# Optimization experiments

Measured on AMD Instinct MI355X. Metric: run time of the kernel, lower is better.

Reference implementation:

```python
import jax, jax.numpy as jnp
import numpy as np

B, S, C = 4, 4096, 1024
H, D, K = 16, 64, 256  # nhead, head_dim, dim_k


def setup_inputs() -> dict:
    key = jax.random.key(0)
    ks = jax.random.split(key, 7)
    x = jax.random.normal(ks[0], (B, S, C), dtype=jnp.float32)
    # per-head QKV projection weights (torch Linear weight layout [out,in])
    Wq = jax.random.normal(ks[1], (H, D, C), dtype=jnp.float32) * (C ** -0.5)
    Wk = jax.random.normal(ks[2], (H, D, C), dtype=jnp.float32) * (C ** -0.5)
    Wv = jax.random.normal(ks[3], (H, D, C), dtype=jnp.float32) * (C ** -0.5)
    # Linformer E/F sequence projections, per head: [K, S]
    We = jax.random.normal(ks[4], (H, K, S), dtype=jnp.float32) * (S ** -0.5)
    Wf = jax.random.normal(ks[5], (H, K, S), dtype=jnp.float32) * (S ** -0.5)
    # output projection (with bias, as w_o is nn.Linear default bias=True)
    Wo = jax.random.normal(ks[6], (C, H * D), dtype=jnp.float32) * ((H * D) ** -0.5)
    bo = jnp.zeros((C,), dtype=jnp.float32)
    return {"x": x, "Wq": Wq, "Wk": Wk, "Wv": Wv, "We": We, "Wf": Wf, "Wo": Wo, "bo": bo}


def reference(x, Wq, Wk, Wv, We, Wf, Wo, bo):
    # per-head projections: [B,H,S,D]
    Q = jnp.einsum('bsc,hdc->bhsd', x, Wq)
    Kh = jnp.einsum('bsc,hdc->bhsd', x, Wk)
    Vh = jnp.einsum('bsc,hdc->bhsd', x, Wv)
    # E-projection of K over the sequence axis: K^T [B,H,D,S] -> [B,H,D,K]
    Kp = jnp.einsum('bhsd,hks->bhdk', Kh, We)
    # scores: Q @ E(K^T) / sqrt(head_dim), softmax over low-rank axis k
    scale = 1.0 / jnp.sqrt(jnp.asarray(D, dtype=x.dtype))
    P = jax.nn.softmax(jnp.einsum('bhsd,bhdk->bhsk', Q, Kp) * scale, axis=-1)
    # F-projection of V over the sequence axis, then transpose back: [B,H,K,D]
    Vp = jnp.einsum('bhsd,hks->bhkd', Vh, Wf)
    out = jnp.einsum('bhsk,bhkd->bhsd', P, Vp)          # [B,H,S,D]
    out = out.transpose(0, 2, 1, 3).reshape(B, S, H * D)  # concat heads
    return jnp.einsum('bse,ce->bsc', out, Wo) + bo       # w_o (dropout=0)
```

## Files before the change

### kernel.cpp

```cpp
#include <hip/hip_runtime.h>
#include <stdint.h>


typedef unsigned short u16;
typedef __bf16 bf16t;
typedef bf16t bf16x8 __attribute__((ext_vector_type(8)));
typedef float f32x4 __attribute__((ext_vector_type(4)));
typedef u16 u16x8 __attribute__((ext_vector_type(8)));

#define MFMA16(a, b, c) __builtin_amdgcn_mfma_f32_16x16x32_bf16((a), (b), (c), 0, 0, 0)

__device__ __forceinline__ u16 f2bf(float f) {
  return __builtin_bit_cast(u16, (bf16t)f);
}

__device__ __forceinline__ bf16x8 ldf(const u16* p) { return *(const bf16x8*)p; }

__device__ __forceinline__ void gload16(const void* g, void* l) {
  __builtin_amdgcn_global_load_lds(
      (__attribute__((address_space(1))) void*)g,
      (__attribute__((address_space(3))) void*)l, 16, 0, 0);
}

__device__ __forceinline__ int xcd_swz(int orig, int nwg) {
  return (orig & 7) * (nwg >> 3) + (orig >> 3);
}

__device__ __forceinline__ void gemm256_pipe(const u16* __restrict__ A,
                                             const u16* __restrict__ B,
                                             int m0, int n0, int sA1, int sB1,
                                             int s0, int kt0, f32x4 acc[8][4],
                                             char* smc) {
  const int tid = threadIdx.x;
  const int w = tid >> 6, l = tid & 63, g = l >> 4, r = l & 15;
  const int wr = w >> 2, wc = w & 3;
  const int lrow = l >> 2;
  const int ksw = (((l & 3) ^ ((l >> 3) & 3)) << 4);
  const int gx = ((g ^ ((r >> 1) & 3)) << 4);

  auto stage = [&](const u16* Base, int r0, int s1, int T, int ch, int ldsoff) {
#pragma unroll
    for (int i = 0; i < 2; ++i) {
      const int row = r0 + (w * 2 + i) * 16 + lrow;
      const size_t eoff = (size_t)(row >> 6) * s1 + (size_t)(row & 63) * s0;
      gload16((const char*)Base + eoff * 2 + ((kt0 + T) * 64 + ch * 32) * 2 + ksw,
              smc + ldsoff + (w * 2 + i) * 1024);
    }
  };

  stage(A, m0, sA1, 0, 0, 0);
  stage(B, n0, sB1, 0, 0, 32768);
  stage(A, m0, sA1, 0, 1, 16384);
  stage(B, n0, sB1, 0, 1, 32768 + 16384);

  for (int t = 0; t < 16; ++t) {
    const int buf = (t & 1) << 16, nb = buf ^ 65536;
    const int Tn = t < 15 ? t + 1 : 15;
    bf16x8 af[4], bfv[4];

#define QUAD(MH)                                                        \
  __builtin_amdgcn_s_setprio(1);                                        \
  _Pragma("unroll") for (int m = 0; m < 4; ++m)                         \
      _Pragma("unroll") for (int n = 0; n < 4; ++n)                     \
          acc[(MH)*4 + m][n] = MFMA16(af[m], bfv[n], acc[(MH)*4 + m][n]); \
  __builtin_amdgcn_s_setprio(0);

    stage(A, m0, sA1, Tn, 0, nb);
    asm volatile("s_waitcnt vmcnt(6)" ::: "memory");
    __builtin_amdgcn_s_barrier();
    asm volatile("" ::: "memory");
    {
      const char* At = smc + buf;
      const char* Bt = smc + buf + 32768;
#pragma unroll
      for (int n = 0; n < 4; ++n)
        bfv[n] = *(const bf16x8*)(Bt + (wc * 64 + n * 16 + r) * 64 + gx);
#pragma unroll
      for (int m = 0; m < 4; ++m)
        af[m] = *(const bf16x8*)(At + (wr * 128 + m * 16 + r) * 64 + gx);
      QUAD(0)
      stage(B, n0, sB1, Tn, 0, nb + 32768);
#pragma unroll
      for (int m = 0; m < 4; ++m)
        af[m] = *(const bf16x8*)(At + (wr * 128 + 64 + m * 16 + r) * 64 + gx);
      QUAD(1)
    }
    stage(A, m0, sA1, Tn, 1, nb + 16384);
    asm volatile("s_waitcnt vmcnt(6)" ::: "memory");
    __builtin_amdgcn_s_barrier();
    asm volatile("" ::: "memory");
    {
      const char* At = smc + buf + 16384;
      const char* Bt = smc + buf + 32768 + 16384;
#pragma unroll
      for (int n = 0; n < 4; ++n)
        bfv[n] = *(const bf16x8*)(Bt + (wc * 64 + n * 16 + r) * 64 + gx);
#pragma unroll
      for (int m = 0; m < 4; ++m)
        af[m] = *(const bf16x8*)(At + (wr * 128 + m * 16 + r) * 64 + gx);
      QUAD(0)
      stage(B, n0, sB1, Tn, 1, nb + 32768 + 16384);
#pragma unroll
      for (int m = 0; m < 4; ++m)
        af[m] = *(const bf16x8*)(At + (wr * 128 + 64 + m * 16 + r) * 64 + gx);
      QUAD(1)
    }
#undef QUAD
  }
}

__global__ __launch_bounds__(256) void cvt_x(const float* __restrict__ src,
                                             u16* __restrict__ dst) {
  const size_t i = ((size_t)blockIdx.x * 256 + threadIdx.x) * 8;
  const float4 a = *(const float4*)(src + i);
  const float4 b = *(const float4*)(src + i + 4);
  u16x8 o;
  o[0] = f2bf(a.x); o[1] = f2bf(a.y); o[2] = f2bf(a.z); o[3] = f2bf(a.w);
  o[4] = f2bf(b.x); o[5] = f2bf(b.y); o[6] = f2bf(b.z); o[7] = f2bf(b.w);
  *(u16x8*)(dst + i) = o;
}

__global__ __launch_bounds__(256) void cvt_w(const float* __restrict__ Wq,
                                             const float* __restrict__ Wk,
                                             const float* __restrict__ Wv,
                                             const float* __restrict__ Wo,
                                             u16* __restrict__ wqkv,
                                             u16* __restrict__ wob) {
  const float* s;
  u16* d;
  switch (blockIdx.y) {
    case 0: s = Wq; d = wqkv; break;
    case 1: s = Wk; d = wqkv + 1048576; break;
    case 2: s = Wv; d = wqkv + 2097152; break;
    default: s = Wo; d = wob; break;
  }
  const size_t i = ((size_t)blockIdx.x * 256 + threadIdx.x) * 8;
  const float4 a = *(const float4*)(s + i);
  const float4 b = *(const float4*)(s + i + 4);
  u16x8 o;
  o[0] = f2bf(a.x); o[1] = f2bf(a.y); o[2] = f2bf(a.z); o[3] = f2bf(a.w);
  o[4] = f2bf(b.x); o[5] = f2bf(b.y); o[6] = f2bf(b.z); o[7] = f2bf(b.w);
  *(u16x8*)(d + i) = o;
}

__global__ __launch_bounds__(256) void cvt_wef(const float* __restrict__ We,
                                               const float* __restrict__ Wf,
                                               u16* __restrict__ web,
                                               u16* __restrict__ wfb) {
  const float* s = blockIdx.y ? Wf : We;
  u16* d = blockIdx.y ? wfb : web;
  const size_t i = ((size_t)blockIdx.x * 256 + threadIdx.x) * 8;
  const float4 a = *(const float4*)(s + i);
  const float4 b = *(const float4*)(s + i + 4);
  u16x8 o;
  o[0] = f2bf(a.x); o[1] = f2bf(a.y); o[2] = f2bf(a.z); o[3] = f2bf(a.w);
  o[4] = f2bf(b.x); o[5] = f2bf(b.y); o[6] = f2bf(b.z); o[7] = f2bf(b.w);
  *(u16x8*)(d + i) = o;
}

__global__ __launch_bounds__(512, 2) void gemm_q(const u16* __restrict__ A,
                                                 const u16* __restrict__ BT,
                                                 u16* __restrict__ Qd) {
  __shared__ u16 sm[65536];
  const int wg = xcd_swz(blockIdx.x, 256);
  const int m0 = (wg >> 2) * 256, n0 = (wg & 3) * 256;
  const int tid = threadIdx.x, w = tid >> 6, l = tid & 63, g = l >> 4, r = l & 15;
  const int wr = w >> 2, wc = w & 3;
  f32x4 acc[8][4] = {};
  gemm256_pipe(A, BT, m0, n0, 65536, 65536, 1024, 0, acc, (char*)sm);
#pragma unroll
  for (int m = 0; m < 8; ++m)
#pragma unroll
    for (int n = 0; n < 4; ++n)
#pragma unroll
      for (int j = 0; j < 4; ++j) {
        const int mm = m0 + wr * 128 + m * 16 + g * 4 + j;
        const int nn = n0 + wc * 64 + n * 16 + r;
        const int b = mm >> 12, s = mm & 4095, h = nn >> 6, d = nn & 63;
        Qd[(((size_t)(b * 16 + h)) * 4096 + s) * 64 + d] = f2bf(acc[m][n][j] * 0.125f);
      }
}

__global__ __launch_bounds__(512, 2) void gemm_kv(const u16* __restrict__ A,
                                                  const u16* __restrict__ BT,
                                                  u16* __restrict__ KTd,
                                                  u16* __restrict__ VTd) {
  __shared__ u16 sm[65536];
  const int wg = xcd_swz(blockIdx.x, 512);
  const int m0 = (wg & 7) * 256, n0 = (wg >> 3) * 256;
  const int tid = threadIdx.x, w = tid >> 6, l = tid & 63, g = l >> 4, r = l & 15;
  const int wr = w >> 2, wc = w & 3;
  f32x4 acc[8][4] = {};
  gemm256_pipe(A, BT, m0, n0, 65536, 65536, 1024, 0, acc, (char*)sm);
#pragma unroll
  for (int m = 0; m < 8; ++m)
#pragma unroll
    for (int n = 0; n < 4; ++n)
#pragma unroll
      for (int j = 0; j < 4; ++j) {
        const int mm = m0 + wr * 128 + m * 16 + g * 4 + j;
        const int nn = n0 + wc * 64 + n * 16 + r;
        const int which = mm >> 10, hd = mm & 1023, h = hd >> 6, d = hd & 63;
        const int b = nn >> 12, s = nn & 4095;
        u16* dst = which ? VTd : KTd;
        dst[(((size_t)(b * 16 + h)) * 64 + d) * 4096 + s] = f2bf(acc[m][n][j]);
      }
}

__global__ __launch_bounds__(512, 2) void gemm_out(const u16* __restrict__ A,
                                                   const u16* __restrict__ BT,
                                                   const float* __restrict__ bo,
                                                   float* __restrict__ out) {
  __shared__ u16 sm[65536];
  const int wg = xcd_swz(blockIdx.x, 256);
  const int m0 = (wg >> 2) * 256, n0 = (wg & 3) * 256;
  const int tid = threadIdx.x, w = tid >> 6, l = tid & 63, g = l >> 4, r = l & 15;
  const int wr = w >> 2, wc = w & 3;
  f32x4 acc[8][4] = {};
  gemm256_pipe(A, BT, m0, n0, 65536, 65536, 1024, 0, acc, (char*)sm);
#pragma unroll
  for (int m = 0; m < 8; ++m)
#pragma unroll
    for (int n = 0; n < 4; ++n)
#pragma unroll
      for (int j = 0; j < 4; ++j) {
        const int mm = m0 + wr * 128 + m * 16 + g * 4 + j;
        const int nn = n0 + wc * 64 + n * 16 + r;
        out[(size_t)mm * 1024 + nn] = acc[m][n][j] + bo[nn];
      }
}

__global__ __launch_bounds__(512, 2) void gemm_small(const u16* __restrict__ web,
                                                     const u16* __restrict__ wfb,
                                                     const u16* __restrict__ KT,
                                                     const u16* __restrict__ VT,
                                                     float* __restrict__ part) {
  __shared__ u16 sm[65536];
  const int bx = blockIdx.x;
  const int h = bx & 15, mode = (bx >> 4) & 1, chunk = bx >> 5;
  const u16 *Ab, *Bb;
  int sA1, sB1;
  if (mode == 0) {
    Ab = web + (size_t)h * 1048576; sA1 = 262144;
    Bb = KT + (size_t)h * 262144;   sB1 = 4194304;
  } else {
    Ab = VT + (size_t)h * 262144;   sA1 = 4194304;
    Bb = wfb + (size_t)h * 1048576; sB1 = 262144;
  }
  f32x4 acc[8][4] = {};
  gemm256_pipe(Ab, Bb, 0, 0, sA1, sB1, 4096, chunk * 16, acc, (char*)sm);
  float* Cp = part + ((size_t)((mode * 4 + chunk) * 16 + h)) * 65536;
  const int tid = threadIdx.x, w = tid >> 6, l = tid & 63, g = l >> 4, r = l & 15;
  const int wr = w >> 2, wc = w & 3;
#pragma unroll
  for (int m = 0; m < 8; ++m)
#pragma unroll
    for (int n = 0; n < 4; ++n)
#pragma unroll
      for (int j = 0; j < 4; ++j)
        Cp[(size_t)(wr * 128 + m * 16 + g * 4 + j) * 256 + wc * 64 + n * 16 + r] =
            acc[m][n][j];
}

__global__ __launch_bounds__(256) void reduce_small(const float* __restrict__ part,
                                                    u16* __restrict__ Kp,
                                                    u16* __restrict__ VpT) {
  const int i = blockIdx.x * 256 + threadIdx.x;
  const int mode = i >> 18;
  const int rem = i & 262143;
  const int h = rem >> 14;
  const int e = (rem & 16383) * 4;
  const int m = e >> 8, n = e & 255;
  const float* pb = part + ((size_t)mode * 64 + h) * 65536 + e;
  const float4 s0 = *(const float4*)(pb);
  const float4 s1 = *(const float4*)(pb + 1048576);
  const float4 s2 = *(const float4*)(pb + 2097152);
  const float4 s3 = *(const float4*)(pb + 3145728);
  ushort4 o;
  o.x = f2bf(s0.x + s1.x + s2.x + s3.x);
  o.y = f2bf(s0.y + s1.y + s2.y + s3.y);
  o.z = f2bf(s0.z + s1.z + s2.z + s3.z);
  o.w = f2bf(s0.w + s1.w + s2.w + s3.w);
  if (mode == 0) {
    const int b = n >> 6, d = n & 63;
    *(ushort4*)(Kp + ((size_t)(b * 16 + h)) * 16384 + m * 64 + d) = o;
  } else {
    const int b = m >> 6, d = m & 63;
    *(ushort4*)(VpT + ((size_t)(b * 16 + h)) * 16384 + d * 256 + n) = o;
  }
}

__global__ __launch_bounds__(256, 1) void attn_fused(const u16* __restrict__ Q,
                                                     const u16* __restrict__ Kp,
                                                     const u16* __restrict__ VpT,
                                                     u16* __restrict__ att) {
  __shared__ u16 P[4][16 * 264];
  const int gid = blockIdx.x;
  const int bh = gid >> 3;
  const int st = gid & 7;
  const int hh = bh & 15, b = bh >> 4;
  const int tid = threadIdx.x, w = tid >> 6, l = tid & 63, g = l >> 4, r = l & 15;
  const u16* Kpb = Kp + (size_t)bh * 256 * 64;
  const u16* Vb = VpT + (size_t)bh * 64 * 256;

  bf16x8 kf[32];
  bf16x8 vf[32];
#pragma unroll
  for (int fn = 0; fn < 16; ++fn) {
    kf[fn * 2 + 0] = ldf(Kpb + (fn * 16 + r) * 64 + g * 8);
    kf[fn * 2 + 1] = ldf(Kpb + (fn * 16 + r) * 64 + 32 + g * 8);
  }
#pragma unroll
  for (int fn2 = 0; fn2 < 4; ++fn2)
#pragma unroll
    for (int kk = 0; kk < 8; ++kk)
      vf[fn2 * 8 + kk] = ldf(Vb + (fn2 * 16 + r) * 256 + kk * 32 + g * 8);

  u16* Pw = P[w];
  for (int t = 0; t < 8; ++t) {
    const int s0 = st * 512 + t * 64 + w * 16;
    const u16* Qb = Q + ((size_t)bh * 4096 + s0) * 64;
    const bf16x8 qf0 = ldf(Qb + r * 64 + g * 8);
    const bf16x8 qf1 = ldf(Qb + r * 64 + 32 + g * 8);
    f32x4 sc[16];
#pragma unroll
    for (int fn = 0; fn < 16; ++fn) {
      sc[fn] = MFMA16(qf0, kf[fn * 2 + 0], (f32x4){});
      sc[fn] = MFMA16(qf1, kf[fn * 2 + 1], sc[fn]);
    }
    float rinv[4];
#pragma unroll
    for (int j = 0; j < 4; ++j) {
      float sum = 0.f;
#pragma unroll
      for (int fn = 0; fn < 16; ++fn) {
        const float e = __expf(sc[fn][j]);
        sc[fn][j] = e;
        sum += e;
      }
      sum += __shfl_xor(sum, 1);
      sum += __shfl_xor(sum, 2);
      sum += __shfl_xor(sum, 4);
      sum += __shfl_xor(sum, 8);
      rinv[j] = 1.0f / sum;
    }
#pragma unroll
    for (int fn = 0; fn < 16; ++fn)
#pragma unroll
      for (int j = 0; j < 4; ++j)
        Pw[(g * 4 + j) * 264 + fn * 16 + r] = f2bf(sc[fn][j]);

    f32x4 o[4] = {};
#pragma unroll
    for (int kk = 0; kk < 8; ++kk) {
      const bf16x8 pa = ldf(Pw + r * 264 + kk * 32 + g * 8);
#pragma unroll
      for (int fn2 = 0; fn2 < 4; ++fn2)
        o[fn2] = MFMA16(pa, vf[fn2 * 8 + kk], o[fn2]);
    }
#pragma unroll
    for (int fn2 = 0; fn2 < 4; ++fn2)
#pragma unroll
      for (int j = 0; j < 4; ++j) {
        const int s = s0 + g * 4 + j;
        const int d = fn2 * 16 + r;
        att[((size_t)b * 4096 + s) * 1024 + hh * 64 + d] = f2bf(o[fn2][j] * rinv[j]);
      }
  }
}

extern "C" void kernel_launch(void* const* d_in, const int* in_sizes, int n_in,
                              void* d_out, int out_size, void* d_ws, size_t ws_size,
                              hipStream_t stream) {
  (void)in_sizes; (void)n_in; (void)out_size; (void)ws_size;
  const float* x  = (const float*)d_in[0];
  const float* Wq = (const float*)d_in[1];
  const float* Wk = (const float*)d_in[2];
  const float* Wv = (const float*)d_in[3];
  const float* We = (const float*)d_in[4];
  const float* Wf = (const float*)d_in[5];
  const float* Wo = (const float*)d_in[6];
  const float* bo = (const float*)d_in[7];
  char* ws = (char*)d_ws;
  u16* xb    = (u16*)(ws + 0);
  float* prt = (float*)(ws + 0);
  u16* att   = (u16*)(ws + 0);
  u16* wqkv  = (u16*)(ws + 33554432);
  u16* web   = (u16*)(ws + 39845888);
  u16* wfb   = (u16*)(ws + 73400320);
  u16* wob   = (u16*)(ws + 106954752);
  u16* Qd    = (u16*)(ws + 109051904);
  u16* KTd   = (u16*)(ws + 142606336);
  u16* VTd   = (u16*)(ws + 176160768);
  u16* Kpd   = (u16*)(ws + 209715200);
  u16* VpTd  = (u16*)(ws + 211812352);

  cvt_x<<<8192, 256, 0, stream>>>(x, xb);
  cvt_w<<<dim3(512, 4), 256, 0, stream>>>(Wq, Wk, Wv, Wo, wqkv, wob);
  cvt_wef<<<dim3(8192, 2), 256, 0, stream>>>(We, Wf, web, wfb);
  gemm_q<<<256, 512, 0, stream>>>(xb, wqkv, Qd);
  gemm_kv<<<512, 512, 0, stream>>>(wqkv + 1048576, xb, KTd, VTd);
  gemm_small<<<128, 512, 0, stream>>>(web, wfb, KTd, VTd, prt);
  reduce_small<<<2048, 256, 0, stream>>>(prt, Kpd, VpTd);
  attn_fused<<<512, 256, 0, stream>>>(Qd, Kpd, VpTd, att);
  gemm_out<<<256, 512, 0, stream>>>(att, wob, bo, (float*)d_out);
}
```

Measured before the change: 322.0 us.

## Restructure GEMM main loop into barrier-separated read/compute phases

Reorders the 256x256 GEMM mainloop so LDS fragment reads are issued before each prefetch stage. Each quarter-MFMA block now sits between barriers, and the vmcnt waits move to after the second-half stage. A full drain plus barrier is added after the prologue. The goal is to keep waves in lockstep, ping-pong style, so LDS reads and global-to-LDS loads overlap MFMA work across waves. The cost is four more barriers per half-iteration, which may add stalls.

```diff
diff --git a/kernel.cpp b/kernel.cpp
--- a/kernel.cpp
+++ b/kernel.cpp
@@ -25,6 +25,14 @@
 __device__ __forceinline__ int xcd_swz(int orig, int nwg) {
   return (orig & 7) * (nwg >> 3) + (orig >> 3);
 }
+
+#define FENCE asm volatile("" ::: "memory")
+#define BAR                                  \
+  do {                                       \
+    FENCE;                                   \
+    __builtin_amdgcn_s_barrier();            \
+    FENCE;                                   \
+  } while (0)
 
 __device__ __forceinline__ void gemm256_pipe(const u16* __restrict__ A,
                                              const u16* __restrict__ B,
@@ -48,65 +56,63 @@
     }
   };
 
+#define RD_B(dst, Bt)                                                     \
+  _Pragma("unroll") for (int n = 0; n < 4; ++n)                           \
+      dst[n] = *(const bf16x8*)((Bt) + (wc * 64 + n * 16 + r) * 64 + gx);
+#define RD_A(dst, At, MH)                                                 \
+  _Pragma("unroll") for (int m = 0; m < 4; ++m)                           \
+      dst[m] = *(const bf16x8*)((At) + (wr * 128 + (MH)*64 + m * 16 + r) * 64 + gx);
+#define QUAD(MH)                                                          \
+  __builtin_amdgcn_s_setprio(1);                                          \
+  _Pragma("unroll") for (int m = 0; m < 4; ++m)                           \
+      _Pragma("unroll") for (int n = 0; n < 4; ++n)                       \
+          acc[(MH)*4 + m][n] = MFMA16(af[m], bfv[n], acc[(MH)*4 + m][n]); \
+  __builtin_amdgcn_s_setprio(0);
+
   stage(A, m0, sA1, 0, 0, 0);
   stage(B, n0, sB1, 0, 0, 32768);
   stage(A, m0, sA1, 0, 1, 16384);
-  stage(B, n0, sB1, 0, 1, 32768 + 16384);
+  stage(B, n0, sB1, 0, 1, 49152);
+  asm volatile("s_waitcnt vmcnt(0)" ::: "memory");
+  BAR;
 
   for (int t = 0; t < 16; ++t) {
     const int buf = (t & 1) << 16, nb = buf ^ 65536;
     const int Tn = t < 15 ? t + 1 : 15;
     bf16x8 af[4], bfv[4];
-
-#define QUAD(MH)                                                        \
-  __builtin_amdgcn_s_setprio(1);                                        \
-  _Pragma("unroll") for (int m = 0; m < 4; ++m)                         \
-      _Pragma("unroll") for (int n = 0; n < 4; ++n)                     \
-          acc[(MH)*4 + m][n] = MFMA16(af[m], bfv[n], acc[(MH)*4 + m][n]); \
-  __builtin_amdgcn_s_setprio(0);
-
+    const char* At0 = smc + buf;
+    const char* Bt0 = smc + buf + 32768;
+    const char* At1 = smc + buf + 16384;
+    const char* Bt1 = smc + buf + 49152;
+
+    RD_B(bfv, Bt0)
+    RD_A(af, At0, 0)
     stage(A, m0, sA1, Tn, 0, nb);
-    asm volatile("s_waitcnt vmcnt(6)" ::: "memory");
-    __builtin_amdgcn_s_barrier();
-    asm volatile("" ::: "memory");
-    {
-      const char* At = smc + buf;
-      const char* Bt = smc + buf + 32768;
-#pragma unroll
-      for (int n = 0; n < 4; ++n)
-        bfv[n] = *(const bf16x8*)(Bt + (wc * 64 + n * 16 + r) * 64 + gx);
-#pragma unroll
-      for (int m = 0; m < 4; ++m)
-        af[m] = *(const bf16x8*)(At + (wr * 128 + m * 16 + r) * 64 + gx);
-      QUAD(0)
-      stage(B, n0, sB1, Tn, 0, nb + 32768);
-#pragma unroll
-      for (int m = 0; m < 4; ++m)
-        af[m] = *(const bf16x8*)(At + (wr * 128 + 64 + m * 16 + r) * 64 + gx);
-      QUAD(1)
-    }
+    BAR;
+    QUAD(0)
+    BAR;
+    RD_A(af, At0, 1)
+    stage(B, n0, sB1, Tn, 0, nb + 32768);
+    asm volatile("s_waitcnt vmcnt(4)" ::: "memory");
+    BAR;
+    QUAD(1)
+    BAR;
+    RD_B(bfv, Bt1)
+    RD_A(af, At1, 0)
     stage(A, m0, sA1, Tn, 1, nb + 16384);
-    asm volatile("s_waitcnt vmcnt(6)" ::: "memory");
-    __builtin_amdgcn_s_barrier();
-    asm volatile("" ::: "memory");
-    {
-      const char* At = smc + buf + 16384;
-      const char* Bt = smc + buf + 32768 + 16384;
-#pragma unroll
-      for (int n = 0; n < 4; ++n)
-        bfv[n] = *(const bf16x8*)(Bt + (wc * 64 + n * 16 + r) * 64 + gx);
-#pragma unroll
-      for (int m = 0; m < 4; ++m)
-        af[m] = *(const bf16x8*)(At + (wr * 128 + m * 16 + r) * 64 + gx);
-      QUAD(0)
-      stage(B, n0, sB1, Tn, 1, nb + 32768 + 16384);
-#pragma unroll
-      for (int m = 0; m < 4; ++m)
-        af[m] = *(const bf16x8*)(At + (wr * 128 + 64 + m * 16 + r) * 64 + gx);
-      QUAD(1)
-    }
+    BAR;
+    QUAD(0)
+    BAR;
+    RD_A(af, At1, 1)
+    stage(B, n0, sB1, Tn, 1, nb + 49152);
+    asm volatile("s_waitcnt vmcnt(4)" ::: "memory");
+    BAR;
+    QUAD(1)
+    BAR;
+  }
+#undef RD_B
+#undef RD_A
 #undef QUAD
-  }
 }
 
 __global__ __launch_bounds__(256) void cvt_x(const float* __restrict__ src,
```

Measured after the change: 324.1 us. Within noise of the previous version (+0.7%).
